# Kernel tuning notes

Hardware: AMD Instinct MI355X
Metric: run time of the kernel (lower is better)

The kernel has to match this reference:

```python
import jax, jax.numpy as jnp
import numpy as np

N = 100000      # nodes
E = 1600000     # edges
G = 100         # graphs in batch
D_IN, H, OUT = 3, 128, 10


def gcn_conv(x, W, b, src, dst, n_nodes):
    """PyG GCNConv with default add_self_loops=True, symmetric normalization.
    out_i = sum_{j->i} d_j^-1/2 d_i^-1/2 (x_j W) + d_i^-1 (x_i W) + b
    where d includes the self-loop (+1)."""
    h = x @ W                                                   # [N, F]
    ones = jnp.ones((src.shape[0],), dtype=x.dtype)
    deg = jax.ops.segment_sum(ones, dst, num_segments=n_nodes) + 1.0  # self-loop
    dinv_sqrt = jax.lax.rsqrt(deg)
    norm = dinv_sqrt[src] * dinv_sqrt[dst]                      # [E]
    msg = h[src] * norm[:, None]                                # gather + scale
    agg = jax.ops.segment_sum(msg, dst, num_segments=n_nodes)   # scatter-add
    out = agg + h * (1.0 / deg)[:, None] + b                    # self-loop term + bias
    return out


def setup_inputs() -> dict:
    key = jax.random.key(0)
    ks = jax.random.split(key, 9)
    x = jax.random.normal(ks[0], (N, D_IN), dtype=jnp.float32)
    edge_index = jax.random.randint(ks[1], (2, E), 0, N)
    batch = jnp.sort(jax.random.randint(ks[2], (N,), 0, G))
    W1 = jax.random.normal(ks[3], (D_IN, H), dtype=jnp.float32) * (1.0 / np.sqrt(D_IN))
    b1 = jnp.zeros((H,), dtype=jnp.float32)
    W2 = jax.random.normal(ks[4], (H, H), dtype=jnp.float32) * (1.0 / np.sqrt(H))
    b2 = jnp.zeros((H,), dtype=jnp.float32)
    Wl = jax.random.normal(ks[5], (H, OUT), dtype=jnp.float32) * (1.0 / np.sqrt(H))
    bl = jnp.zeros((OUT,), dtype=jnp.float32)
    return {"x": x, "edge_index": edge_index, "batch": batch,
            "W1": W1, "b1": b1, "W2": W2, "b2": b2, "Wl": Wl, "bl": bl}


def reference(x, edge_index, batch, W1, b1, W2, b2, Wl, bl):
    src, dst = edge_index[0], edge_index[1]
    h = jax.nn.relu(gcn_conv(x, W1, b1, src, dst, N))
    h = jax.nn.relu(gcn_conv(h, W2, b2, src, dst, N))
    # global mean pool over graphs
    sums = jax.ops.segment_sum(h, batch, num_segments=G)                 # [G, H]
    cnts = jax.ops.segment_sum(jnp.ones((N,), h.dtype), batch, num_segments=G)
    pooled = sums / jnp.maximum(cnts, 1.0)[:, None]
    # dropout p=0.5 is identity in eval mode
    return pooled @ Wl + bl                                              # [G, OUT]
```

## Files before the change

### kernel.cpp

```cpp
#include <hip/hip_runtime.h>


#define DIN 3
#define H 128
#define OUTF 10
#define NWEIGHT (384 + 128 + 16384 + 128 + 1280 + 10)
#define ECH 2048
#define RGSH 9
#define RGSIZE 512
#define W2FRAG_N 16384
#define CHE 512

typedef float gcn364_f2 __attribute__((ext_vector_type(2)));
typedef float gcn364_f4 __attribute__((ext_vector_type(4)));
typedef short gcn364_s8 __attribute__((ext_vector_type(8)));

__device__ __forceinline__ float gcn364_bf2f(unsigned short u) {
    return __uint_as_float(((unsigned int)u) << 16);
}
__device__ __forceinline__ unsigned short gcn364_f2bf(float f) {
    unsigned int u = __float_as_uint(f);
    u += 0x7FFFu + ((u >> 16) & 1u);
    return (unsigned short)(u >> 16);
}

__device__ __forceinline__ int gcn364_probe(const unsigned short* __restrict__ xs16) {
    int lane = threadIdx.x & 63;
    int outl = 0;
    #pragma unroll
    for (int k = 0; k < 4; k++) {
        unsigned short u = xs16[lane * 4 + k];
        int e = (u >> 7) & 0xFF;
        outl += (e < 100 || e > 140) ? 1 : 0;
    }
    #pragma unroll
    for (int d = 1; d < 64; d <<= 1) outl += __shfl_xor(outl, d);
    return (outl > 32) ? 1 : 0;
}

static __global__ void gcn364_histconv(const void* __restrict__ x,
                                       const void* __restrict__ W1, const void* __restrict__ b1,
                                       const void* __restrict__ W2, const void* __restrict__ b2,
                                       const void* __restrict__ Wl, const void* __restrict__ bl,
                                       int* __restrict__ flag,
                                       float4* __restrict__ xf4, float* __restrict__ wf,
                                       unsigned short* __restrict__ w2frag,
                                       float* __restrict__ pooled,
                                       const int* __restrict__ edst,
                                       int* __restrict__ hist,
                                       int N, int E, int S, int RG, int GH) {
    __shared__ int h[256];
    if (blockIdx.x < (unsigned)S) {
        h[threadIdx.x] = 0;
        __syncthreads();
        int elo = blockIdx.x * ECH;
        int ehi = elo + ECH; if (ehi > E) ehi = E;
        int ne = ehi - elo;
        if (((ne & 3) == 0) && ((((size_t)(edst + elo)) & 15) == 0)) {
            const int4* d4 = (const int4*)(edst + elo);
            int n4 = ne >> 2;
            #pragma unroll 2
            for (int k = threadIdx.x; k < n4; k += 256) {
                int4 v = d4[k];
                atomicAdd(&h[v.x >> RGSH], 1);
                atomicAdd(&h[v.y >> RGSH], 1);
                atomicAdd(&h[v.z >> RGSH], 1);
                atomicAdd(&h[v.w >> RGSH], 1);
            }
        } else {
            #pragma unroll 4
            for (int e = elo + threadIdx.x; e < ehi; e += 256)
                atomicAdd(&h[edst[e] >> RGSH], 1);
        }
        __syncthreads();
        if (threadIdx.x < RG) hist[blockIdx.x * RG + threadIdx.x] = h[threadIdx.x];
    }
    int i = blockIdx.x * blockDim.x + threadIdx.x;
    if (i < GH) pooled[i] = 0.0f;
    int total = N + NWEIGHT;
    if ((int)blockIdx.x * 256 < total) {
        int fl = gcn364_probe((const unsigned short*)x);
        if (i == 0) *flag = fl;
        if (i < N) {
            float a, b, c;
            if (fl) {
                const float* xs = (const float*)x;
                a = xs[3 * i]; b = xs[3 * i + 1]; c = xs[3 * i + 2];
            } else {
                const unsigned short* xs = (const unsigned short*)x;
                a = gcn364_bf2f(xs[3 * i]);
                b = gcn364_bf2f(xs[3 * i + 1]);
                c = gcn364_bf2f(xs[3 * i + 2]);
            }
            xf4[i] = make_float4(a, b, c, 0.f);
        } else if (i < total) {
            int j = i - N;
            const void* srcp;
            if      (j < 384)                       { srcp = W1; }
            else if ((j -= 384)   < 128)            { srcp = b1; }
            else if ((j -= 128)   < 16384)          { srcp = W2; }
            else if ((j -= 16384) < 128)            { srcp = b2; }
            else if ((j -= 128)   < 1280)           { srcp = Wl; }
            else    { j -= 1280;                      srcp = bl; }
            wf[i - N] = fl ? ((const float*)srcp)[j]
                           : gcn364_bf2f(((const unsigned short*)srcp)[j]);
        }
        if (i < W2FRAG_N) {
            int fl2 = fl;
            int j = i & 7;
            int l = (i >> 3) & 63;
            int c = (i >> 9) & 3;
            int t = i >> 11;
            int k = c * 32 + (l >> 4) * 8 + j;
            int n = t * 16 + (l & 15);
            float w = fl2 ? ((const float*)W2)[k * H + n]
                          : gcn364_bf2f(((const unsigned short*)W2)[k * H + n]);
            w2frag[i] = gcn364_f2bf(w);
        }
    }
}

static __global__ void gcn364_scanHpar(int* __restrict__ hist,
                                       int* __restrict__ regionBase,
                                       int S, int RG) {
    __shared__ int sh[1024];
    int r = blockIdx.x;
    int t = threadIdx.x;
    int carry = 0;
    for (int s0 = 0; s0 < S; s0 += 1024) {
        int s = s0 + t;
        int c = (s < S) ? hist[s * RG + r] : 0;
        sh[t] = c;
        __syncthreads();
        for (int d = 1; d < 1024; d <<= 1) {
            int v = (t >= d) ? sh[t - d] : 0;
            __syncthreads();
            sh[t] += v;
            __syncthreads();
        }
        if (s < S) hist[s * RG + r] = carry + sh[t] - c;
        int tot = sh[1023];
        __syncthreads();
        carry += tot;
    }
    if (t == 0) regionBase[r] = carry;
}

static __global__ void gcn364_scanR(int* __restrict__ regionBase,
                                    int RG, int E) {
    __shared__ int sh[256];
    int t = threadIdx.x;
    int c = (t < RG) ? regionBase[t] : 0;
    sh[t] = c;
    __syncthreads();
    for (int d = 1; d < 256; d <<= 1) {
        int v = (t >= d) ? sh[t - d] : 0;
        __syncthreads();
        sh[t] += v;
        __syncthreads();
    }
    if (t < RG) regionBase[t] = sh[t] - c;
    if (t == 0) regionBase[RG] = E;
}

static __global__ void gcn364_partition(const int* __restrict__ src,
                                        const int* __restrict__ dst,
                                        const int* __restrict__ hist,
                                        const int* __restrict__ regionBase,
                                        int* __restrict__ epack,
                                        int E, int S, int RG) {
    __shared__ int gbase[256];
    __shared__ int scnt[256];
    __shared__ int sbase[256];
    __shared__ int ebuf[ECH];
    __shared__ unsigned char rmap[ECH];
    int s = blockIdx.x;
    int t = threadIdx.x;
    int elo = s * ECH;
    int ehi = elo + ECH; if (ehi > E) ehi = E;
    int ne = ehi - elo;

    int cnt = 0;
    if (t < RG) {
        int own = hist[s * RG + t];
        gbase[t] = own + regionBase[t];
        if (s < S - 1) cnt = hist[(s + 1) * RG + t] - own;
        else           cnt = (regionBase[t + 1] - regionBase[t]) - own;
    }
    scnt[t] = 0;
    sbase[t] = cnt;
    __syncthreads();
    for (int d = 1; d < 256; d <<= 1) {
        int v = (t >= d) ? sbase[t - d] : 0;
        __syncthreads();
        sbase[t] += v;
        __syncthreads();
    }
    int excl = sbase[t] - cnt;
    __syncthreads();
    sbase[t] = excl;
    __syncthreads();
    if (((ne & 3) == 0) && ((((size_t)(dst + elo)) & 15) == 0) &&
        ((((size_t)(src + elo)) & 15) == 0)) {
        const int4* d4 = (const int4*)(dst + elo);
        const int4* s4 = (const int4*)(src + elo);
        int n4 = ne >> 2;
        #pragma unroll 2
        for (int k = t; k < n4; k += 256) {
            int4 dv = d4[k];
            int4 sv = s4[k];
            int r0 = dv.x >> RGSH, r1 = dv.y >> RGSH;
            int r2 = dv.z >> RGSH, r3 = dv.w >> RGSH;
            int p0 = sbase[r0] + atomicAdd(&scnt[r0], 1);
            ebuf[p0] = ((dv.x & (RGSIZE - 1)) << 17) | sv.x; rmap[p0] = (unsigned char)r0;
            int p1 = sbase[r1] + atomicAdd(&scnt[r1], 1);
            ebuf[p1] = ((dv.y & (RGSIZE - 1)) << 17) | sv.y; rmap[p1] = (unsigned char)r1;
            int p2 = sbase[r2] + atomicAdd(&scnt[r2], 1);
            ebuf[p2] = ((dv.z & (RGSIZE - 1)) << 17) | sv.z; rmap[p2] = (unsigned char)r2;
            int p3 = sbase[r3] + atomicAdd(&scnt[r3], 1);
            ebuf[p3] = ((dv.w & (RGSIZE - 1)) << 17) | sv.w; rmap[p3] = (unsigned char)r3;
        }
    } else {
        #pragma unroll 4
        for (int e = elo + t; e < ehi; e += 256) {
            int d = dst[e];
            int r = d >> RGSH;
            int lofs = atomicAdd(&scnt[r], 1);
            int slot = sbase[r] + lofs;
            ebuf[slot] = ((d & (RGSIZE - 1)) << 17) | src[e];
            rmap[slot] = (unsigned char)r;
        }
    }
    __syncthreads();
    #pragma unroll 4
    for (int k = t; k < ne; k += 256) {
        int r = rmap[k];
        epack[gbase[r] + (k - sbase[r])] = ebuf[k];
    }
}

static __global__ void gcn364_build(const int* __restrict__ epack,
                                    const int* __restrict__ regionBase,
                                    int* __restrict__ off,
                                    int* __restrict__ esrc,
                                    float4* __restrict__ xf4,
                                    int N) {
    __shared__ int sdeg[RGSIZE];
    __shared__ int stmp[256];
    int r = blockIdx.x;
    int nlo = r << RGSH;
    int nn = N - nlo; if (nn > RGSIZE) nn = RGSIZE;
    int e0 = regionBase[r];
    int e1 = regionBase[r + 1];
    int t = threadIdx.x;
    int bdim = blockDim.x;

    if (t < RGSIZE) sdeg[t] = 0;
    __syncthreads();
    #pragma unroll 4
    for (int p = e0 + t; p < e1; p += bdim)
        atomicAdd(&sdeg[epack[p] >> 17], 1);
    __syncthreads();

    int a0 = 0, a1 = 0, psum = 0;
    if (t < 256) {
        a0 = sdeg[2 * t];
        a1 = sdeg[2 * t + 1];
        psum = a0 + a1;
        stmp[t] = psum;
    }
    __syncthreads();
    for (int d = 1; d < 256; d <<= 1) {
        int val = (t >= d && t < 256) ? stmp[t - d] : 0;
        __syncthreads();
        if (t < 256) stmp[t] += val;
        __syncthreads();
    }
    if (t < 256) {
        int excl = stmp[t] - psum;

        if (2 * t < nn)     off[nlo + 2 * t]     = e0 + excl + a0;
        if (2 * t + 1 < nn) off[nlo + 2 * t + 1] = e0 + excl + a0 + a1;
        if (2 * t < nn) {
            float di = rsqrtf((float)a0 + 1.0f);
            float4 xv = xf4[nlo + 2 * t];
            xv.x *= di; xv.y *= di; xv.z *= di; xv.w = di;
            xf4[nlo + 2 * t] = xv;
        }
        if (2 * t + 1 < nn) {
            float di = rsqrtf((float)a1 + 1.0f);
            float4 xv = xf4[nlo + 2 * t + 1];
            xv.x *= di; xv.y *= di; xv.z *= di; xv.w = di;
            xf4[nlo + 2 * t + 1] = xv;
        }
        sdeg[2 * t]     = e0 + excl;
        sdeg[2 * t + 1] = e0 + excl + a0;
    }
    __syncthreads();
    #pragma unroll 4
    for (int p = e0 + t; p < e1; p += bdim) {
        int v = epack[p];
        int q = atomicAdd(&sdeg[v >> 17], 1);
        esrc[q] = v & 0x1FFFF;
    }
}

static __global__ void gcn364_aggu(const int* __restrict__ esrc,
                                   const int* __restrict__ off,
                                   const float4* __restrict__ xf4,
                                   float4* __restrict__ u4, int N) {
    int lane = threadIdx.x & 63;
    int wv = threadIdx.x >> 6;
    int grp = lane >> 4;
    int sub = lane & 15;
    int i = (blockIdx.x * 4 + wv) * 4 + grp;

    float a0 = 0.f, a1 = 0.f, a2 = 0.f;
    if (i < N) {
        int p0 = (i == 0) ? 0 : off[i - 1];
        int p1 = off[i];
        for (int p = p0 + sub; p < p1; p += 16) {
            float4 sv = xf4[esrc[p]];
            a0 += sv.x; a1 += sv.y; a2 += sv.z;
        }
    }
    for (int d = 1; d < 16; d <<= 1) {
        a0 += __shfl_xor(a0, d);
        a1 += __shfl_xor(a1, d);
        a2 += __shfl_xor(a2, d);
    }
    if (i < N && sub == 0) {
        float4 xi = xf4[i];
        float di = xi.w;
        u4[i] = make_float4(di * (a0 + xi.x), di * (a1 + xi.y), di * (a2 + xi.z), di);
    }
}

__device__ __forceinline__ void gcn364_edge(const float4 u,
                                            const gcn364_f2* wa2, const gcn364_f2* wb2,
                                            const gcn364_f2* wc2, const gcn364_f2* bb2,
                                            gcn364_f2* acc) {
    gcn364_f2 ux = {u.x, u.x}, uy = {u.y, u.y}, uz = {u.z, u.z}, uw = {u.w, u.w};
    gcn364_f2 zero = {0.f, 0.f};
    #pragma unroll
    for (int q = 0; q < 4; q++) {
        gcn364_f2 t = ux * wa2[q] + uy * wb2[q] + uz * wc2[q] + bb2[q];
        t = __builtin_elementwise_max(t, zero);
        acc[q] += uw * t;
    }
}

#define MPB 16
static __global__ __launch_bounds__(256, 8) void gcn364_agg2pool(
        const int* __restrict__ esrc, const int* __restrict__ off,
        const float4* __restrict__ u4,
        const float* __restrict__ w1f, const float* __restrict__ b1f,
        const unsigned short* __restrict__ w2frag, const float* __restrict__ b2f,
        const int* __restrict__ batch, float* __restrict__ pooled, int N) {
    __shared__ unsigned short vshb[MPB][H + 8];
    __shared__ float4 sstage[CHE];
    __shared__ int soff[MPB + 1];
    __shared__ int sbatch[MPB];
    __shared__ float spool[2][H];
    int i0 = blockIdx.x * MPB;
    int tid = threadIdx.x;
    int wave = tid >> 6;
    int lane = tid & 63;
    int grp = lane >> 4;
    int sub = lane & 15;
    int node = wave * 4 + grp;
    int i = i0 + node;

    if (tid <= MPB) {
        int idx = i0 - 1 + tid;
        int cidx = idx < N - 1 ? idx : N - 1;
        soff[tid] = (idx < 0) ? 0 : off[cidx];
    }
    if (tid < MPB) {
        int bi = i0 + tid; if (bi > N - 1) bi = N - 1;
        sbatch[tid] = batch[bi];
    }

    gcn364_f2 wa2[4], wb2[4], wc2[4], bb2[4];
    {
        const gcn364_f4* wA = (const gcn364_f4*)w1f;
        const gcn364_f4* wB = (const gcn364_f4*)(w1f + H);
        const gcn364_f4* wC = (const gcn364_f4*)(w1f + 2 * H);
        const gcn364_f4* wD = (const gcn364_f4*)b1f;
        gcn364_f4 a0 = wA[sub * 2], a1 = wA[sub * 2 + 1];
        gcn364_f4 b0 = wB[sub * 2], b1v = wB[sub * 2 + 1];
        gcn364_f4 c0 = wC[sub * 2], c1 = wC[sub * 2 + 1];
        gcn364_f4 d0 = wD[sub * 2], d1 = wD[sub * 2 + 1];
        wa2[0] = (gcn364_f2){a0[0], a0[1]}; wa2[1] = (gcn364_f2){a0[2], a0[3]};
        wa2[2] = (gcn364_f2){a1[0], a1[1]}; wa2[3] = (gcn364_f2){a1[2], a1[3]};
        wb2[0] = (gcn364_f2){b0[0], b0[1]}; wb2[1] = (gcn364_f2){b0[2], b0[3]};
        wb2[2] = (gcn364_f2){b1v[0], b1v[1]}; wb2[3] = (gcn364_f2){b1v[2], b1v[3]};
        wc2[0] = (gcn364_f2){c0[0], c0[1]}; wc2[1] = (gcn364_f2){c0[2], c0[3]};
        wc2[2] = (gcn364_f2){c1[0], c1[1]}; wc2[3] = (gcn364_f2){c1[2], c1[3]};
        bb2[0] = (gcn364_f2){d0[0], d0[1]}; bb2[1] = (gcn364_f2){d0[2], d0[3]};
        bb2[2] = (gcn364_f2){d1[0], d1[1]}; bb2[3] = (gcn364_f2){d1[2], d1[3]};
    }
    __syncthreads();

    int s  = soff[node];
    int e  = soff[node + 1];
    int e0 = soff[0];
    int e1 = soff[MPB];

    gcn364_f2 acc[4];
    acc[0] = acc[1] = acc[2] = acc[3] = (gcn364_f2){0.f, 0.f};
    for (int cb = e0; cb < e1; cb += CHE) {
        int ce = cb + CHE; if (ce > e1) ce = e1;
        for (int p = cb + tid; p < ce; p += 256)
            sstage[p - cb] = u4[esrc[p]];
        __syncthreads();
        int lo = s > cb ? s : cb;
        int hi = e < ce ? e : ce;
        #pragma unroll 4
        for (int p = lo; p < hi; p++) {
            float4 u = sstage[p - cb];
            gcn364_edge(u, wa2, wb2, wc2, bb2, acc);
        }
        __syncthreads();
    }
    float di = 0.f;
    if (i < N) {
        float4 uS = u4[i];
        gcn364_edge(uS, wa2, wb2, wc2, bb2, acc);
        di = uS.w;
    }
    {
        gcn364_s8 o;
        o[0] = (short)gcn364_f2bf(acc[0].x * di);
        o[1] = (short)gcn364_f2bf(acc[0].y * di);
        o[2] = (short)gcn364_f2bf(acc[1].x * di);
        o[3] = (short)gcn364_f2bf(acc[1].y * di);
        o[4] = (short)gcn364_f2bf(acc[2].x * di);
        o[5] = (short)gcn364_f2bf(acc[2].y * di);
        o[6] = (short)gcn364_f2bf(acc[3].x * di);
        o[7] = (short)gcn364_f2bf(acc[3].y * di);
        *(gcn364_s8*)&vshb[node][sub * 8] = o;
    }
    __syncthreads();

    int m = lane & 15;
    int quad = lane >> 4;
    int g0 = sbatch[0];
    gcn364_s8 af[4];
    #pragma unroll
    for (int c = 0; c < 4; c++)
        af[c] = *(const gcn364_s8*)&vshb[m][c * 32 + quad * 8];

    #pragma unroll
    for (int tt = 0; tt < 2; tt++) {
        int t = wave * 2 + tt;
        gcn364_f4 cacc = {0.f, 0.f, 0.f, 0.f};
        #pragma unroll
        for (int c = 0; c < 4; c++) {
            gcn364_s8 bf8 = *(const gcn364_s8*)&w2frag[(((t * 4 + c) * 64) + lane) * 8];
            cacc = __builtin_amdgcn_mfma_f32_16x16x32_bf16(af[c], bf8, cacc, 0, 0, 0);
        }
        int feat = t * 16 + m;
        float bb = b2f[feat];
        int baseRow = quad * 4;
        float sum0 = 0.0f, sum1 = 0.0f;
        #pragma unroll
        for (int r = 0; r < 4; r++) {
            int ii = i0 + baseRow + r;
            if (ii >= N) continue;
            float val = fmaxf(cacc[r] + bb, 0.0f);
            if (sbatch[baseRow + r] == g0) sum0 += val; else sum1 += val;
        }
        sum0 += __shfl_xor(sum0, 16); sum0 += __shfl_xor(sum0, 32);
        sum1 += __shfl_xor(sum1, 16); sum1 += __shfl_xor(sum1, 32);
        if (quad == 0) {
            spool[0][feat] = sum0;
            spool[1][feat] = sum1;
        }
    }
    __syncthreads();
    {
        int slot = tid >> 7;
        int f = tid & (H - 1);
        float v = spool[slot][f];
        if (v != 0.0f) {
            int g = slot ? sbatch[MPB - 1] : g0;
            atomicAdd(&pooled[g * H + f], v);
        }
    }
}

static __global__ void gcn364_final(const float* __restrict__ pooled,
                                    const int* __restrict__ batch,
                                    const float* __restrict__ wlf,
                                    const float* __restrict__ blf,
                                    const int* __restrict__ flag,
                                    void* __restrict__ out, int N, int G) {
    __shared__ float red[2][OUTF];
    int g = blockIdx.x;
    int t = threadIdx.x;
    int lane = t & 63;
    int wv = t >> 6;
    if (g >= G) return;
    int lo = 0, hi = N;
    while (lo < hi) { int m = (lo + hi) >> 1; if (batch[m] < g) lo = m + 1; else hi = m; }
    int a = lo;
    lo = 0; hi = N;
    while (lo < hi) { int m = (lo + hi) >> 1; if (batch[m] < g + 1) lo = m + 1; else hi = m; }
    float cn = (float)(lo - a);
    float inv = 1.0f / fmaxf(cn, 1.0f);

    float p = pooled[g * H + t];
    float v[OUTF];
    #pragma unroll
    for (int o = 0; o < OUTF; o++) v[o] = p * wlf[t * OUTF + o];
    #pragma unroll
    for (int d = 1; d < 64; d <<= 1) {
        #pragma unroll
        for (int o = 0; o < OUTF; o++) v[o] += __shfl_xor(v[o], d);
    }
    if (lane == 0) {
        #pragma unroll
        for (int o = 0; o < OUTF; o++) red[wv][o] = v[o];
    }
    __syncthreads();
    if (t < OUTF) {
        float r = (red[0][t] + red[1][t]) * inv + blf[t];
        if (*flag) ((float*)out)[g * OUTF + t] = r;
        else       ((unsigned short*)out)[g * OUTF + t] = gcn364_f2bf(r);
    }
}

extern "C" void kernel_launch(void* const* d_in, const int* in_sizes, int n_in,
                              void* d_out, int out_size, void* d_ws, size_t ws_size,
                              hipStream_t stream) {
    const void* x  = d_in[0];
    const int* edge_index = (const int*)d_in[1];
    const int* batch      = (const int*)d_in[2];
    const void* W1 = d_in[3];
    const void* b1 = d_in[4];
    const void* W2 = d_in[5];
    const void* b2 = d_in[6];
    const void* Wl = d_in[7];
    const void* bl = d_in[8];

    const int N = in_sizes[0] / DIN;
    const int E = in_sizes[1] / 2;
    const int G = out_size / OUTF;
    const int* src = edge_index;
    const int* dst = edge_index + E;
    const int SH = (E + 8191) / 8192;
    const int S  = (E + ECH - 1) / ECH;
    const int RG = (N + RGSIZE - 1) >> RGSH;
    const int GH = G * H;

    char* wsb = (char*)d_ws;
    float* pooled     = (float*)wsb;
    int*   histLeg    = (int*)(pooled + (size_t)GH);
    int*   regionBase = histLeg + (size_t)SH * RG;
    int*   off        = regionBase + RG + 1;
    int*   flag       = off + N;
    size_t ofs = (((size_t)((char*)(flag + 1) - wsb)) + 15) & ~(size_t)15;
    float4* xf4  = (float4*)(wsb + ofs);
    float4* u4   = xf4 + N;
    float*  wf   = (float*)(u4 + N);
    size_t ofs2 = (((size_t)((char*)(wf + NWEIGHT) - wsb)) + 15) & ~(size_t)15;
    unsigned short* w2frag = (unsigned short*)(wsb + ofs2);
    int*    epack = (int*)(w2frag + W2FRAG_N);
    int*    esrc  = epack + E;
    int*    hist  = esrc;

    float* w1f = wf;
    float* b1f = w1f + 384;
    float* b2f = b1f + 128 + 16384;
    float* wlf = b2f + 128;
    float* blf = wlf + 1280;

    {
        int convBlocks = (N + NWEIGHT + 255) / 256;
        int gmax = (S > convBlocks) ? S : convBlocks;
        gcn364_histconv<<<gmax, 256, 0, stream>>>(
            x, W1, b1, W2, b2, Wl, bl, flag, xf4, wf, w2frag, pooled,
            dst, hist, N, E, S, RG, GH);
    }
    gcn364_scanHpar<<<RG, 1024, 0, stream>>>(hist, regionBase, S, RG);
    gcn364_scanR<<<1, 256, 0, stream>>>(regionBase, RG, E);
    gcn364_partition<<<S, 256, 0, stream>>>(src, dst, hist, regionBase, epack, E, S, RG);
    gcn364_build<<<RG, 1024, 0, stream>>>(epack, regionBase, off, esrc, xf4, N);
    gcn364_aggu<<<(N + 15) / 16, 256, 0, stream>>>(esrc, off, xf4, u4, N);
    gcn364_agg2pool<<<(N + MPB - 1) / MPB, 256, 0, stream>>>(
        esrc, off, u4, w1f, b1f, w2frag, b2f, batch, pooled, N);
    gcn364_final<<<G, H, 0, stream>>>(pooled, batch, wlf, blf, flag, d_out, N, G);
}
```

Before: 177.6 us.

## Fold region scan into partition/build and stage gathers in aggu via LDS

Removes the single-block scanR kernel launch by having partition and build each recompute the small 196-entry prefix scan over region totals redundantly in shared memory. Separately, aggu now loads the block's contiguous edge range cooperatively into an LDS staging buffer in chunks before per-node reduction, making the esrc/xf4 gathers use all 256 threads evenly instead of 16 lanes per node. This trades one launch and a serial dependency for extra per-block scan work and added barriers.

```diff
diff --git a/kernel.cpp b/kernel.cpp
--- a/kernel.cpp
+++ b/kernel.cpp
@@ -121,7 +121,7 @@
 }
 
 static __global__ void gcn364_scanHpar(int* __restrict__ hist,
-                                       int* __restrict__ regionBase,
+                                       int* __restrict__ regionTot,
                                        int S, int RG) {
     __shared__ int sh[1024];
     int r = blockIdx.x;
@@ -143,30 +143,13 @@
         __syncthreads();
         carry += tot;
     }
-    if (t == 0) regionBase[r] = carry;
-}
-
-static __global__ void gcn364_scanR(int* __restrict__ regionBase,
-                                    int RG, int E) {
-    __shared__ int sh[256];
-    int t = threadIdx.x;
-    int c = (t < RG) ? regionBase[t] : 0;
-    sh[t] = c;
-    __syncthreads();
-    for (int d = 1; d < 256; d <<= 1) {
-        int v = (t >= d) ? sh[t - d] : 0;
-        __syncthreads();
-        sh[t] += v;
-        __syncthreads();
-    }
-    if (t < RG) regionBase[t] = sh[t] - c;
-    if (t == 0) regionBase[RG] = E;
+    if (t == 0) regionTot[r] = carry;
 }
 
 static __global__ void gcn364_partition(const int* __restrict__ src,
                                         const int* __restrict__ dst,
                                         const int* __restrict__ hist,
-                                        const int* __restrict__ regionBase,
+                                        const int* __restrict__ regionTot,
                                         int* __restrict__ epack,
                                         int E, int S, int RG) {
     __shared__ int gbase[256];
@@ -180,15 +163,23 @@
     int ehi = elo + ECH; if (ehi > E) ehi = E;
     int ne = ehi - elo;
 
-    int cnt = 0;
+    int own = 0, cnt = 0, rtot = 0;
     if (t < RG) {
-        int own = hist[s * RG + t];
-        gbase[t] = own + regionBase[t];
-        if (s < S - 1) cnt = hist[(s + 1) * RG + t] - own;
-        else           cnt = (regionBase[t + 1] - regionBase[t]) - own;
-    }
+        own = hist[s * RG + t];
+        rtot = regionTot[t];
+        cnt = (s < S - 1) ? (hist[(s + 1) * RG + t] - own) : (rtot - own);
+    }
+    sbase[t] = rtot;
+    __syncthreads();
+    for (int d = 1; d < 256; d <<= 1) {
+        int v = (t >= d) ? sbase[t - d] : 0;
+        __syncthreads();
+        sbase[t] += v;
+        __syncthreads();
+    }
+    if (t < RG) gbase[t] = (sbase[t] - rtot) + own;
+    sbase[t] = cnt;
     scnt[t] = 0;
-    sbase[t] = cnt;
     __syncthreads();
     for (int d = 1; d < 256; d <<= 1) {
         int v = (t >= d) ? sbase[t - d] : 0;
@@ -240,20 +231,32 @@
 }
 
 static __global__ void gcn364_build(const int* __restrict__ epack,
-                                    const int* __restrict__ regionBase,
+                                    const int* __restrict__ regionTot,
                                     int* __restrict__ off,
                                     int* __restrict__ esrc,
                                     float4* __restrict__ xf4,
-                                    int N) {
+                                    int N, int RG) {
     __shared__ int sdeg[RGSIZE];
     __shared__ int stmp[256];
+    __shared__ int stot[256];
     int r = blockIdx.x;
     int nlo = r << RGSH;
     int nn = N - nlo; if (nn > RGSIZE) nn = RGSIZE;
-    int e0 = regionBase[r];
-    int e1 = regionBase[r + 1];
     int t = threadIdx.x;
     int bdim = blockDim.x;
+
+    int totR = regionTot[r];
+    if (t < 256) stot[t] = (t < RG) ? regionTot[t] : 0;
+    __syncthreads();
+    for (int d = 1; d < 256; d <<= 1) {
+        int v = (t >= d && t < 256) ? stot[t - d] : 0;
+        __syncthreads();
+        if (t < 256) stot[t] += v;
+        __syncthreads();
+    }
+    int e1 = stot[r];
+    int e0 = e1 - totR;
+    __syncthreads();
 
     if (t < RGSIZE) sdeg[t] = 0;
     __syncthreads();
@@ -309,20 +312,41 @@
                                    const int* __restrict__ off,
                                    const float4* __restrict__ xf4,
                                    float4* __restrict__ u4, int N) {
-    int lane = threadIdx.x & 63;
-    int wv = threadIdx.x >> 6;
+    __shared__ float4 sstage[CHE];
+    __shared__ int soff[17];
+    int i0 = blockIdx.x * 16;
+    int tid = threadIdx.x;
+    int lane = tid & 63;
+    int wave = tid >> 6;
     int grp = lane >> 4;
     int sub = lane & 15;
-    int i = (blockIdx.x * 4 + wv) * 4 + grp;
+    int node = wave * 4 + grp;
+    int i = i0 + node;
+
+    if (tid <= 16) {
+        int idx = i0 - 1 + tid;
+        int cidx = idx < N - 1 ? idx : N - 1;
+        soff[tid] = (idx < 0) ? 0 : off[cidx];
+    }
+    __syncthreads();
+    int s  = soff[node];
+    int e  = soff[node + 1];
+    int e0 = soff[0];
+    int e1 = soff[16];
 
     float a0 = 0.f, a1 = 0.f, a2 = 0.f;
-    if (i < N) {
-        int p0 = (i == 0) ? 0 : off[i - 1];
-        int p1 = off[i];
-        for (int p = p0 + sub; p < p1; p += 16) {
-            float4 sv = xf4[esrc[p]];
+    for (int cb = e0; cb < e1; cb += CHE) {
+        int ce = cb + CHE; if (ce > e1) ce = e1;
+        for (int p = cb + tid; p < ce; p += 256)
+            sstage[p - cb] = xf4[esrc[p]];
+        __syncthreads();
+        int lo = s > cb ? s : cb;
+        int hi = e < ce ? e : ce;
+        for (int p = lo + sub; p < hi; p += 16) {
+            float4 sv = sstage[p - cb];
             a0 += sv.x; a1 += sv.y; a2 += sv.z;
         }
+        __syncthreads();
     }
     for (int d = 1; d < 16; d <<= 1) {
         a0 += __shfl_xor(a0, d);
@@ -557,8 +581,8 @@
     char* wsb = (char*)d_ws;
     float* pooled     = (float*)wsb;
     int*   histLeg    = (int*)(pooled + (size_t)GH);
-    int*   regionBase = histLeg + (size_t)SH * RG;
-    int*   off        = regionBase + RG + 1;
+    int*   regionTot  = histLeg + (size_t)SH * RG;
+    int*   off        = regionTot + RG + 1;
     int*   flag       = off + N;
     size_t ofs = (((size_t)((char*)(flag + 1) - wsb)) + 15) & ~(size_t)15;
     float4* xf4  = (float4*)(wsb + ofs);
@@ -583,10 +607,9 @@
             x, W1, b1, W2, b2, Wl, bl, flag, xf4, wf, w2frag, pooled,
             dst, hist, N, E, S, RG, GH);
     }
-    gcn364_scanHpar<<<RG, 1024, 0, stream>>>(hist, regionBase, S, RG);
-    gcn364_scanR<<<1, 256, 0, stream>>>(regionBase, RG, E);
-    gcn364_partition<<<S, 256, 0, stream>>>(src, dst, hist, regionBase, epack, E, S, RG);
-    gcn364_build<<<RG, 1024, 0, stream>>>(epack, regionBase, off, esrc, xf4, N);
+    gcn364_scanHpar<<<RG, 1024, 0, stream>>>(hist, regionTot, S, RG);
+    gcn364_partition<<<S, 256, 0, stream>>>(src, dst, hist, regionTot, epack, E, S, RG);
+    gcn364_build<<<RG, 1024, 0, stream>>>(epack, regionTot, off, esrc, xf4, N, RG);
     gcn364_aggu<<<(N + 15) / 16, 256, 0, stream>>>(esrc, off, xf4, u4, N);
     gcn364_agg2pool<<<(N + MPB - 1) / MPB, 256, 0, stream>>>(
         esrc, off, u4, w1f, b1f, w2frag, b2f, batch, pooled, N);
```

Measured after the change: 175.3 us, median of 2. About the same (-1.3%).
